# Kernel tuning notes

Measured on AMD Instinct MI355X. Metric: run time of the kernel, lower is better.

Reference implementation:

```python
import jax, jax.numpy as jnp
import numpy as np

B, T, C, H, D, E, K = 4, 1024, 1024, 16, 64, 8, 2
HID = 2 * D  # expert MLP hidden width (assumed 2*head_dim)
NEG = jnp.finfo(jnp.float32).min


def setup_inputs() -> dict:
    key = jax.random.key(0)
    ks = jax.random.split(key, 16)
    s = 0.02
    # rotary tables [max_pos, head_dim]
    inv_freq = 1.0 / (10000.0 ** (jnp.arange(0, D, 2, dtype=jnp.float32) / D))
    freqs = jnp.arange(T, dtype=jnp.float32)[:, None] * inv_freq[None, :]
    emb = jnp.concatenate([freqs, freqs], axis=-1)  # [T, D]
    return {
        "x": jax.random.normal(ks[0], (B, T, C), jnp.float32),
        "position_ids": jnp.sort(jax.random.randint(ks[1], (B, T), 0, T), axis=-1),
        "cos": jnp.cos(emb),
        "sin": jnp.sin(emb),
        "rq": s * jax.random.normal(ks[2], (D, E), jnp.float32),
        "rk": s * jax.random.normal(ks[3], (D, E), jnp.float32),
        "rv": s * jax.random.normal(ks[4], (D, E), jnp.float32),
        "q_w1": s * jax.random.normal(ks[5], (E, D, HID), jnp.float32),
        "q_w2": s * jax.random.normal(ks[6], (E, HID, D), jnp.float32),
        "k_w1": s * jax.random.normal(ks[7], (E, D, HID), jnp.float32),
        "k_w2": s * jax.random.normal(ks[8], (E, HID, D), jnp.float32),
        "v_w1": s * jax.random.normal(ks[9], (E, D, HID), jnp.float32),
        "v_w2": s * jax.random.normal(ks[10], (E, HID, D), jnp.float32),
        "o_w": s * jax.random.normal(ks[11], (C, C), jnp.float32),  # torch Linear weight [out,in]
    }


def _rotate_half(x):
    x1, x2 = x[..., : D // 2], x[..., D // 2:]
    return jnp.concatenate([-x2, x1], axis=-1)


def _moe_head_proj(xh, r_w, w1, w2):
    """Per-head top-k routed expert MLP. xh: [B,T,H,D]."""
    logits = jnp.einsum('bthd,de->bthe', xh, r_w)            # router logits
    vals, idx = jax.lax.top_k(logits, K)                     # [B,T,H,K]
    w = jax.nn.softmax(vals, axis=-1)
    onehot = jax.nn.one_hot(idx, E, dtype=xh.dtype)          # [B,T,H,K,E]
    w_full = jnp.einsum('bthk,bthke->bthe', w, onehot)       # scatter weights to all experts
    h = jax.nn.gelu(jnp.einsum('bthd,edf->bthef', xh, w1))   # all-expert hidden
    out = jnp.einsum('bthe,bthef,efg->bthg', w_full, h, w2)  # masked weighted combine
    return out, logits


def reference(x, position_ids, cos, sin, rq, rk, rv, q_w1, q_w2, k_w1, k_w2, v_w1, v_w2, o_w):
    xh = x.reshape(B, T, H, D)
    q, _ = _moe_head_proj(xh, rq, q_w1, q_w2)
    k, _ = _moe_head_proj(xh, rk, k_w1, k_w2)
    v, _ = _moe_head_proj(xh, rv, v_w1, v_w2)
    q = q.transpose(0, 2, 1, 3)  # [B,H,T,D]
    k = k.transpose(0, 2, 1, 3)
    v = v.transpose(0, 2, 1, 3)
    # RoPE
    c = cos[position_ids][:, None, :, :]  # [B,1,T,D]
    s = sin[position_ids][:, None, :, :]
    q = q * c + _rotate_half(q) * s
    k = k * c + _rotate_half(k) * s
    # causal SDPA
    scores = jnp.einsum('bhqd,bhkd->bhqk', q, k) / jnp.sqrt(jnp.float32(D))
    causal = jnp.tril(jnp.ones((T, T), dtype=bool))
    scores = jnp.where(causal, scores, NEG)
    attn = jax.nn.softmax(scores, axis=-1)
    out = jnp.einsum('bhqk,bhkd->bhqd', attn, v)
    out = out.transpose(0, 2, 1, 3).reshape(B, T, C)
    return out @ o_w.T
```

## Files before the change

kernel.cpp:

```cpp
#include <hip/hip_runtime.h>
#include <math.h>

#define BB 4
#define TT 1024
#define CCH 1024
#define HH 16
#define DD 64
#define EE 8
#define HID 128
#define CAP 8192
#define GEXP 504

typedef unsigned short u16;
typedef unsigned int u32;
typedef short bf16x8 __attribute__((ext_vector_type(8)));
typedef short bf16x4 __attribute__((ext_vector_type(4)));
typedef float f32x4 __attribute__((ext_vector_type(4)));

__device__ __forceinline__ u16 f2bf(float f) {
    unsigned int u = __float_as_uint(f);
    unsigned int r = (u + 0x7FFFu + ((u >> 16) & 1u)) >> 16;
    return (u16)r;
}
__device__ __forceinline__ u16 f2bf_f(float f) {
    return (u16)((__float_as_uint(f) + 0x8000u) >> 16);
}
__device__ __forceinline__ u32 pkbf(float lo, float hi) {
    u32 a = __float_as_uint(lo) + 0x8000u;
    u32 b = __float_as_uint(hi) + 0x8000u;
    return __builtin_amdgcn_perm(b, a, 0x07060302u);
}
__device__ __forceinline__ float gelu_fast(float z) {
    float t = z * z;
    float wn = __builtin_fmaf(t, -0.07135481283f, -1.5957691216f);
    float e = __expf(z * wn);
    return __fdividef(z, 1.f + e);
}

#define GLD16(gp, lp) __builtin_amdgcn_global_load_lds( \
    (const __attribute__((address_space(1))) u32*)(gp), \
    (__attribute__((address_space(3))) u32*)(lp), 16, 0, 0)

__global__ __launch_bounds__(256) void prep_kernel(
    const float* __restrict__ x,
    const float* __restrict__ rq, const float* __restrict__ rk, const float* __restrict__ rv,
    unsigned int* __restrict__ counts,
    unsigned int* __restrict__ idxbuf, float2* __restrict__ wtbuf,
    const float* __restrict__ qw1, const float* __restrict__ kw1, const float* __restrict__ vw1,
    const float* __restrict__ qw2, const float* __restrict__ kw2, const float* __restrict__ vw2,
    u16* __restrict__ img1, u16* __restrict__ img2,
    const float* __restrict__ ow, u16* __restrict__ owbf)
{
    const int bi = blockIdx.x;
    const int tid = threadIdx.x;

    if (bi < 192) {
        int t = bi * 256 + tid;
        if (t < 24576) {
            int c = t & 7, f = (t >> 3) & 127, e = (t >> 10) & 7, p = t >> 13;
            const float* w1 = ((p == 0) ? qw1 : (p == 1) ? kw1 : vw1) + e * 8192;
            int dbase = 8 * (c ^ (f & 7));
            u16 tmp[8];
            #pragma unroll
            for (int j = 0; j < 8; ++j) tmp[j] = f2bf(w1[(dbase + j) * 128 + f]);
            uint4 ov;
            ov.x = (u32)tmp[0] | ((u32)tmp[1] << 16);
            ov.y = (u32)tmp[2] | ((u32)tmp[3] << 16);
            ov.z = (u32)tmp[4] | ((u32)tmp[5] << 16);
            ov.w = (u32)tmp[6] | ((u32)tmp[7] << 16);
            ((uint4*)img1)[t] = ov;
        } else {
            int i = t - 24576;
            int m = i & 15, g = (i >> 4) & 63, e = (i >> 10) & 7, p = i >> 13;
            const float* w2 = ((p == 0) ? qw2 : (p == 1) ? kw2 : vw2) + e * 8192;
            u16* dstrow = img2 + (p * 8 + e) * 8192 + g * 128;
            #pragma unroll
            for (int u = 0; u < 2; ++u) {
                int gg = 2 * m + u;
                int fbase = 16 * (gg >> 2) + 4 * (gg & 3);
                int pos = gg ^ (g & 31);
                u16 a0 = f2bf(w2[(fbase + 0) * 64 + g]);
                u16 a1 = f2bf(w2[(fbase + 1) * 64 + g]);
                u16 a2 = f2bf(w2[(fbase + 2) * 64 + g]);
                u16 a3 = f2bf(w2[(fbase + 3) * 64 + g]);
                uint2 ov;
                ov.x = (u32)a0 | ((u32)a1 << 16);
                ov.y = (u32)a2 | ((u32)a3 << 16);
                *(uint2*)(dstrow + pos * 4) = ov;
            }
        }
        return;
    }

    if (bi < 1216) {
        int i = (bi - 192) * 256 + tid;
        float4 v = ((const float4*)ow)[i];
        unsigned int lov = (unsigned int)f2bf(v.x) | ((unsigned int)f2bf(v.y) << 16);
        unsigned int hiv = (unsigned int)f2bf(v.z) | ((unsigned int)f2bf(v.w) << 16);
        ((uint2*)owbf)[i] = make_uint2(lov, hiv);
        return;
    }

    {
        const unsigned int g = (bi - 1216) * 256 + tid;

        __shared__ float rS[3][64][8];
        __shared__ int lcnt[192];
        __shared__ int lbase[192];

        for (int i = tid; i < 1536; i += 256) {
            int p = i >> 9, rem = i & 511;
            const float* rp = (p == 0) ? rq : (p == 1) ? rk : rv;
            rS[p][rem >> 3][rem & 7] = rp[rem];
        }
        if (tid < 192) lcnt[tid] = 0;
        __syncthreads();

        float lg[3][8];
        #pragma unroll
        for (int p = 0; p < 3; ++p)
            #pragma unroll
            for (int e = 0; e < 8; ++e) lg[p][e] = 0.f;

        const float* xr = x + (size_t)g * 64;
        for (int i4 = 0; i4 < 16; ++i4) {
            float4 xv = ((const float4*)xr)[i4];
            float xa[4] = {xv.x, xv.y, xv.z, xv.w};
            #pragma unroll
            for (int m = 0; m < 4; ++m) {
                int d = i4 * 4 + m;
                #pragma unroll
                for (int p = 0; p < 3; ++p) {
                    float4 r0 = *(const float4*)&rS[p][d][0];
                    float4 r1 = *(const float4*)&rS[p][d][4];
                    lg[p][0] += xa[m] * r0.x; lg[p][1] += xa[m] * r0.y;
                    lg[p][2] += xa[m] * r0.z; lg[p][3] += xa[m] * r0.w;
                    lg[p][4] += xa[m] * r1.x; lg[p][5] += xa[m] * r1.y;
                    lg[p][6] += xa[m] * r1.z; lg[p][7] += xa[m] * r1.w;
                }
            }
        }

        int ppe[3]; float2 pw[3]; int slot[3];
        #pragma unroll
        for (int p = 0; p < 3; ++p) {
            int i1 = 0; float v1 = lg[p][0];
            #pragma unroll
            for (int e = 1; e < 8; ++e) { if (lg[p][e] > v1) { v1 = lg[p][e]; i1 = e; } }
            int i2 = -1; float v2 = -3.402823466e38f;
            #pragma unroll
            for (int e = 0; e < 8; ++e) { if (e != i1 && lg[p][e] > v2) { v2 = lg[p][e]; i2 = e; } }
            float z = __expf(v2 - v1);
            float inv = 1.f / (1.f + z);
            float wa = inv, wb = z * inv;
            int lo = min(i1, i2), hi = max(i1, i2);
            float wlo = (i1 < i2) ? wa : wb;
            float whi = (i1 < i2) ? wb : wa;
            int pel = p * 64 + lo * 8 + hi;
            ppe[p] = pel; pw[p] = make_float2(wlo, whi);
            slot[p] = atomicAdd(&lcnt[pel], 1);
        }
        __syncthreads();
        if (tid < 192) {
            int c = lcnt[tid];
            lbase[tid] = c ? (int)atomicAdd(&counts[tid], (unsigned int)c) : 0;
        }
        __syncthreads();
        #pragma unroll
        for (int p = 0; p < 3; ++p) {
            int pos = lbase[ppe[p]] + slot[p];
            if (pos < CAP) {
                idxbuf[ppe[p] * CAP + pos] = g;
                wtbuf[ppe[p] * CAP + pos]  = pw[p];
            }
        }
    }
}

__global__ __launch_bounds__(128) void sched_kernel(
    const unsigned int* __restrict__ counts, unsigned int* __restrict__ blockinfo)
{
    const int tid = threadIdx.x;
    __shared__ int nsub[84];
    __shared__ int extra[84];
    __shared__ int frac[84];
    __shared__ int alloc[84];
    __shared__ int startS[84];
    __shared__ int nnzS, totalS, rem2S;

    if (tid < 84) {
        int p = tid / 28, q = tid - 28 * p, lo = 0;
        while (q >= 7 - lo) { q -= 7 - lo; ++lo; }
        int hi = lo + 1 + q;
        int n = (int)counts[p * 64 + lo * 8 + hi];
        if (n > CAP) n = CAP;
        nsub[tid] = (n + 31) >> 5;
    }
    __syncthreads();
    if (tid == 0) {
        int tot = 0, nz = 0;
        for (int i = 0; i < 84; ++i) { tot += nsub[i]; nz += (nsub[i] > 0); }
        totalS = tot; nnzS = nz;
    }
    __syncthreads();
    const int R = GEXP - nnzS;
    if (tid < 84) {
        if (nsub[tid] > 0) {
            int e = (int)(((long long)nsub[tid] * R) / totalS);
            extra[tid] = e;
            frac[tid] = nsub[tid] * R - e * totalS;
        } else { extra[tid] = 0; frac[tid] = -1; }
    }
    __syncthreads();
    if (tid == 0) {
        int se = 0;
        for (int i = 0; i < 84; ++i) se += extra[i];
        rem2S = GEXP - nnzS - se;
    }
    __syncthreads();
    if (tid < 84) {
        if (nsub[tid] > 0) {
            int rank = 0;
            for (int j = 0; j < 84; ++j)
                if (nsub[j] > 0 && (frac[j] > frac[tid] || (frac[j] == frac[tid] && j < tid))) ++rank;
            alloc[tid] = 1 + extra[tid] + (rank < rem2S ? 1 : 0);
        } else alloc[tid] = 0;
    }
    __syncthreads();
    if (tid == 0) {
        int s = 0;
        for (int i = 0; i < 84; ++i) { startS[i] = s; s += alloc[i]; }
    }
    __syncthreads();
    if (tid < 84) {
        int a = alloc[tid], st = startS[tid];
        for (int c = 0; c < a; ++c)
            blockinfo[st + c] = (unsigned)tid | ((unsigned)c << 8) | ((unsigned)a << 20);
    }
}

__global__ __launch_bounds__(512, 2) void expert_kernel(
    const float* __restrict__ x, const int* __restrict__ pos_ids,
    const float* __restrict__ cosb, const float* __restrict__ sinb,
    const u16* __restrict__ img1, const u16* __restrict__ img2,
    const unsigned int* __restrict__ counts,
    const unsigned int* __restrict__ idxbuf, const float2* __restrict__ wtbuf,
    const unsigned int* __restrict__ blockinfo,
    u16* __restrict__ qb, u16* __restrict__ kb, u16* __restrict__ vb)
{
    const int tid = threadIdx.x;
    const unsigned int info = blockinfo[blockIdx.x];
    const int pe84 = info & 255;
    const int chunk = (info >> 8) & 0xFFF;
    const int nch = info >> 20;
    const int p = pe84 / 28;
    int q28 = pe84 - p * 28;
    int lo = 0;
    while (q28 >= 7 - lo) { q28 -= 7 - lo; ++lo; }
    const int hi = lo + 1 + q28;
    const int pe = p * 64 + lo * 8 + hi;

    int n = (int)counts[pe]; if (n == 0) return; if (n > CAP) n = CAP;

    u16* outp = (p == 0) ? qb : (p == 1) ? kb : vb;
    const unsigned int* il = idxbuf + pe * CAP;
    const float2* wl = wtbuf + pe * CAP;

    __shared__ __align__(16) u16 wsh[32768];

    {
        const u16* a0 = img1 + (p * 8 + lo) * 8192;
        const u16* b0 = img2 + (p * 8 + lo) * 8192;
        const u16* a1 = img1 + (p * 8 + hi) * 8192;
        const u16* b1 = img2 + (p * 8 + hi) * 8192;
        #pragma unroll
        for (int k = 0; k < 2; ++k) {
            int o = (k * 512 + tid) * 8;
            GLD16(a0 + o, wsh + o);
            GLD16(b0 + o, wsh + 8192 + o);
            GLD16(a1 + o, wsh + 16384 + o);
            GLD16(b1 + o, wsh + 24576 + o);
        }
    }
    __syncthreads();

    const int lane = tid & 63, w = tid >> 6, quad = lane >> 4, m16 = lane & 15;
    const int f7 = m16 & 7;
    const int wid = chunk * 8 + w;
    const int WRK = nch * 8;
    const int nsub = (n + 31) >> 5;

    for (int s = wid; s < nsub; s += WRK) {
        const int base = s * 32;
        unsigned int gtok = 0, obase = 0; float wlo_ = 0.f, whi_ = 0.f;
        int posv = 0, valid = 0;
        if (lane < 32) {
            int j = base + lane;
            valid = (j < n);
            int jc = valid ? j : (n - 1);
            gtok = il[jc];
            float2 wv = wl[jc];
            wlo_ = valid ? wv.x : 0.f; whi_ = valid ? wv.y : 0.f;
            unsigned int b_ = gtok >> 14, h_ = gtok & 15, t_ = (gtok >> 4) & 1023;
            obase = ((b_ * 16 + h_) * 1024 + t_) * 64;
            posv = pos_ids[b_ * 1024 + t_];
        }

        float wf00 = __shfl(wlo_, m16, 64);
        float wf10 = __shfl(whi_, m16, 64);
        float wf01 = __shfl(wlo_, 16 + m16, 64);
        float wf11 = __shfl(whi_, 16 + m16, 64);

        bf16x8 Afr[2][2];
        #pragma unroll
        for (int mt2 = 0; mt2 < 2; ++mt2) {
            unsigned int gm = (unsigned int)__shfl((int)gtok, mt2 * 16 + m16, 64);
            const float* xr = x + (size_t)gm * 64 + 8 * quad;
            float4 xa0 = *(const float4*)(xr);
            float4 xa1 = *(const float4*)(xr + 4);
            float4 xb0 = *(const float4*)(xr + 32);
            float4 xb1 = *(const float4*)(xr + 36);
            bf16x8 A0, A1;
            A0[0] = (short)f2bf_f(xa0.x); A0[1] = (short)f2bf_f(xa0.y);
            A0[2] = (short)f2bf_f(xa0.z); A0[3] = (short)f2bf_f(xa0.w);
            A0[4] = (short)f2bf_f(xa1.x); A0[5] = (short)f2bf_f(xa1.y);
            A0[6] = (short)f2bf_f(xa1.z); A0[7] = (short)f2bf_f(xa1.w);
            A1[0] = (short)f2bf_f(xb0.x); A1[1] = (short)f2bf_f(xb0.y);
            A1[2] = (short)f2bf_f(xb0.z); A1[3] = (short)f2bf_f(xb0.w);
            A1[4] = (short)f2bf_f(xb1.x); A1[5] = (short)f2bf_f(xb1.y);
            A1[6] = (short)f2bf_f(xb1.z); A1[7] = (short)f2bf_f(xb1.w);
            Afr[mt2][0] = A0; Afr[mt2][1] = A1;
        }

        f32x4 acc2[2][4];
        #pragma unroll
        for (int mt2 = 0; mt2 < 2; ++mt2)
            #pragma unroll
            for (int nt = 0; nt < 4; ++nt) acc2[mt2][nt] = (f32x4){0.f, 0.f, 0.f, 0.f};

        #pragma unroll 1
        for (int ekk = 0; ekk < 8; ++ekk) {
            const int e = ekk >> 2;
            const int kk = ekk & 3;
            const u16* w1b = wsh + e * 16384;
            const u16* w2b = w1b + 8192;
            const float wt0 = e ? wf10 : wf00;
            const float wt1 = e ? wf11 : wf01;

            f32x4 c[2][2];
            #pragma unroll
            for (int ntl = 0; ntl < 2; ++ntl) {
                const int f = 16 * (2 * kk + ntl) + m16;
                const u16* w1f = w1b + f * 64;
                bf16x8 wa = *(const bf16x8*)(w1f + (((quad    ) ^ f7) << 3));
                bf16x8 wb = *(const bf16x8*)(w1f + (((quad + 4) ^ f7) << 3));
                #pragma unroll
                for (int mt2 = 0; mt2 < 2; ++mt2) {
                    f32x4 t = (f32x4){0.f, 0.f, 0.f, 0.f};
                    t = __builtin_amdgcn_mfma_f32_16x16x32_bf16(wa, Afr[mt2][0], t, 0, 0, 0);
                    c[ntl][mt2] = __builtin_amdgcn_mfma_f32_16x16x32_bf16(wb, Afr[mt2][1], t, 0, 0, 0);
                }
            }

            bf16x4 w2f[2][4];
            #pragma unroll
            for (int ntl = 0; ntl < 2; ++ntl) {
                const int gg = 4 * (2 * kk + ntl) + quad;
                #pragma unroll
                for (int nt2 = 0; nt2 < 4; ++nt2) {
                    const int g = 16 * nt2 + m16;
                    const int pos = gg ^ (g & 31);
                    w2f[ntl][nt2] = *(const bf16x4*)(w2b + g * 128 + pos * 4);
                }
            }

            #pragma unroll
            for (int mt2 = 0; mt2 < 2; ++mt2) {
                const float wt = mt2 ? wt1 : wt0;
                #pragma unroll
                for (int ntl = 0; ntl < 2; ++ntl) {
                    float g0 = wt * gelu_fast(c[ntl][mt2][0]);
                    float g1 = wt * gelu_fast(c[ntl][mt2][1]);
                    float g2 = wt * gelu_fast(c[ntl][mt2][2]);
                    float g3 = wt * gelu_fast(c[ntl][mt2][3]);
                    union { u32 u[2]; bf16x4 v; } bf_;
                    bf_.u[0] = pkbf(g0, g1);
                    bf_.u[1] = pkbf(g2, g3);
                    #pragma unroll
                    for (int nt2 = 0; nt2 < 4; ++nt2)
                        acc2[mt2][nt2] = __builtin_amdgcn_mfma_f32_16x16x16bf16_1k(
                            w2f[ntl][nt2], bf_.v, acc2[mt2][nt2], 0, 0, 0);
                }
            }
        }

        #pragma unroll
        for (int mt2 = 0; mt2 < 2; ++mt2) {
            const int tk = mt2 * 16 + m16;
            int   pos_r = __shfl(posv, tk, 64);
            unsigned int ob = (unsigned int)__shfl((int)obase, tk, 64);
            int   val_r = __shfl(valid, tk, 64);
            if (p < 2) {
                #pragma unroll
                for (int ntp = 0; ntp < 2; ++ntp) {
                    const int d0 = 16 * ntp + 4 * quad;
                    float4 cv = *(const float4*)&cosb[pos_r * 64 + d0];
                    float4 sv = *(const float4*)&sinb[pos_r * 64 + d0];
                    float o1[4], o2[4];
                    #pragma unroll
                    for (int r = 0; r < 4; ++r) {
                        float v1 = acc2[mt2][ntp][r];
                        float v2 = acc2[mt2][ntp + 2][r];
                        float cd = (&cv.x)[r], sd = (&sv.x)[r];
                        o1[r] = v1 * cd - v2 * sd;
                        o2[r] = v2 * cd + v1 * sd;
                    }
                    if (val_r) {
                        uint2 s1, s2;
                        s1.x = (u32)f2bf(o1[0]) | ((u32)f2bf(o1[1]) << 16);
                        s1.y = (u32)f2bf(o1[2]) | ((u32)f2bf(o1[3]) << 16);
                        s2.x = (u32)f2bf(o2[0]) | ((u32)f2bf(o2[1]) << 16);
                        s2.y = (u32)f2bf(o2[2]) | ((u32)f2bf(o2[3]) << 16);
                        *(uint2*)&outp[ob + d0]      = s1;
                        *(uint2*)&outp[ob + d0 + 32] = s2;
                    }
                }
            } else {
                if (val_r) {
                    #pragma unroll
                    for (int nt2 = 0; nt2 < 4; ++nt2) {
                        uint2 s1;
                        s1.x = (u32)f2bf(acc2[mt2][nt2][0]) | ((u32)f2bf(acc2[mt2][nt2][1]) << 16);
                        s1.y = (u32)f2bf(acc2[mt2][nt2][2]) | ((u32)f2bf(acc2[mt2][nt2][3]) << 16);
                        *(uint2*)&outp[ob + 16 * nt2 + 4 * quad] = s1;
                    }
                }
            }
        }
    }
}

__global__ __launch_bounds__(256) void attn_kernel(
    const u16* __restrict__ qbp, const u16* __restrict__ kbp,
    const u16* __restrict__ vbp, u16* __restrict__ ao)
{
    const int tid = threadIdx.x;
    const int i8 = blockIdx.x & 7;
    const int plane_i = blockIdx.x >> 3;
    const int h = plane_i & 15, b = plane_i >> 4;
    const size_t plane = (size_t)plane_i * 1024 * 64;
    const u16* qp = qbp + plane;
    const u16* kp = kbp + plane;
    const u16* vp = vbp + plane;

    const int w = tid >> 6, lane = tid & 63, quad = lane >> 4, m16 = lane & 15;
    const int row = tid >> 2, seg = tid & 3;
    const int kjv = tid & 63, dgv = tid >> 6;

    __shared__ u16 Ks[64][72];
    __shared__ u16 Vt[64][72];
    __shared__ u16 Ps[4][16][72];

    #pragma unroll 1
    for (int half = 0; half < 2; ++half) {
        const int qt = half ? (15 - i8) : i8;
        const int q0 = qt * 64;

        const u16* qrow = &qp[(size_t)(q0 + 16 * w + m16) * 64 + 8 * quad];
        bf16x8 aq0 = *(const bf16x8*)(qrow);
        bf16x8 aq1 = *(const bf16x8*)(qrow + 32);

        uint4 kr0, kr1; ushort4 vr0, vr1, vr2, vr3;
        {
            const uint4* src = (const uint4*)&kp[(size_t)row * 64 + seg * 16];
            kr0 = src[0]; kr1 = src[1];
            const u16* vb2 = &vp[(size_t)kjv * 64 + dgv * 4];
            vr0 = *(const ushort4*)(vb2);
            vr1 = *(const ushort4*)(vb2 + 16);
            vr2 = *(const ushort4*)(vb2 + 32);
            vr3 = *(const ushort4*)(vb2 + 48);
        }

        float m_s = -1e30f, l_s = 0.f;
        f32x4 oacc[4];
        #pragma unroll
        for (int i = 0; i < 4; ++i) oacc[i] = (f32x4){0.f, 0.f, 0.f, 0.f};

        const int qrow_l = 16 * w + m16;

        for (int kt = 0; kt <= qt; ++kt) {
            __syncthreads();
            {
                uint4* dst = (uint4*)&Ks[row][seg * 16];
                dst[0] = kr0; dst[1] = kr1;
                int d0 = dgv * 4;
                Vt[d0 + 0][kjv] = vr0.x; Vt[d0 + 1][kjv] = vr0.y;
                Vt[d0 + 2][kjv] = vr0.z; Vt[d0 + 3][kjv] = vr0.w;
                Vt[d0 + 16][kjv] = vr1.x; Vt[d0 + 17][kjv] = vr1.y;
                Vt[d0 + 18][kjv] = vr1.z; Vt[d0 + 19][kjv] = vr1.w;
                Vt[d0 + 32][kjv] = vr2.x; Vt[d0 + 33][kjv] = vr2.y;
                Vt[d0 + 34][kjv] = vr2.z; Vt[d0 + 35][kjv] = vr2.w;
                Vt[d0 + 48][kjv] = vr3.x; Vt[d0 + 49][kjv] = vr3.y;
                Vt[d0 + 50][kjv] = vr3.z; Vt[d0 + 51][kjv] = vr3.w;
            }
            __syncthreads();
            if (kt < qt) {
                const int k0n = (kt + 1) * 64;
                const uint4* src = (const uint4*)&kp[(size_t)(k0n + row) * 64 + seg * 16];
                kr0 = src[0]; kr1 = src[1];
                const u16* vb2 = &vp[(size_t)(k0n + kjv) * 64 + dgv * 4];
                vr0 = *(const ushort4*)(vb2);
                vr1 = *(const ushort4*)(vb2 + 16);
                vr2 = *(const ushort4*)(vb2 + 32);
                vr3 = *(const ushort4*)(vb2 + 48);
            }

            f32x4 sv[4];
            #pragma unroll
            for (int ct = 0; ct < 4; ++ct) {
                bf16x8 bk0 = *(const bf16x8*)&Ks[16 * ct + m16][8 * quad];
                bf16x8 bk1 = *(const bf16x8*)&Ks[16 * ct + m16][32 + 8 * quad];
                f32x4 acc = (f32x4){0.f, 0.f, 0.f, 0.f};
                acc = __builtin_amdgcn_mfma_f32_16x16x32_bf16(bk0, aq0, acc, 0, 0, 0);
                acc = __builtin_amdgcn_mfma_f32_16x16x32_bf16(bk1, aq1, acc, 0, 0, 0);
                sv[ct] = acc;
            }

            float s[4][4];
            const bool diag = (kt == qt);
            #pragma unroll
            for (int ct = 0; ct < 4; ++ct)
                #pragma unroll
                for (int reg = 0; reg < 4; ++reg) {
                    float v = sv[ct][reg] * 0.125f;
                    if (diag) {
                        int krow = 16 * ct + 4 * quad + reg;
                        if (krow > qrow_l) v = -1e30f;
                    }
                    s[ct][reg] = v;
                }

            float rm = s[0][0];
            #pragma unroll
            for (int ct = 0; ct < 4; ++ct)
                #pragma unroll
                for (int reg = 0; reg < 4; ++reg) rm = fmaxf(rm, s[ct][reg]);
            rm = fmaxf(rm, __shfl_xor(rm, 16, 64));
            rm = fmaxf(rm, __shfl_xor(rm, 32, 64));
            float mn = fmaxf(m_s, rm);
            float al = __expf(m_s - mn);
            float sum = 0.f;
            #pragma unroll
            for (int ct = 0; ct < 4; ++ct)
                #pragma unroll
                for (int reg = 0; reg < 4; ++reg) {
                    float pv = __expf(s[ct][reg] - mn);
                    s[ct][reg] = pv;
                    sum += pv;
                }
            sum += __shfl_xor(sum, 16, 64);
            sum += __shfl_xor(sum, 32, 64);
            l_s = l_s * al + sum;
            m_s = mn;

            bf16x4 pt[4];
            #pragma unroll
            for (int ct = 0; ct < 4; ++ct) {
                union { u32 u[2]; bf16x4 v; } pb;
                pb.u[0] = pkbf(s[ct][0], s[ct][1]);
                pb.u[1] = pkbf(s[ct][2], s[ct][3]);
                pt[ct] = pb.v;
            }

            #pragma unroll
            for (int dt = 0; dt < 4; ++dt)
                #pragma unroll
                for (int reg = 0; reg < 4; ++reg) oacc[dt][reg] *= al;

            #pragma unroll
            for (int dt = 0; dt < 4; ++dt) {
                #pragma unroll
                for (int ct = 0; ct < 4; ++ct) {
                    bf16x4 vf = *(const bf16x4*)&Vt[16 * dt + m16][16 * ct + 4 * quad];
                    oacc[dt] = __builtin_amdgcn_mfma_f32_16x16x16bf16_1k(vf, pt[ct], oacc[dt], 0, 0, 0);
                }
            }
        }

        float linv = 1.f / l_s;
        #pragma unroll
        for (int dt = 0; dt < 4; ++dt) {
            u32 lo = (u32)f2bf(oacc[dt][0] * linv) | ((u32)f2bf(oacc[dt][1] * linv) << 16);
            u32 hi = (u32)f2bf(oacc[dt][2] * linv) | ((u32)f2bf(oacc[dt][3] * linv) << 16);
            *(u32*)&Ps[w][m16][16 * dt + 4 * quad]     = lo;
            *(u32*)&Ps[w][m16][16 * dt + 4 * quad + 2] = hi;
        }
        __syncthreads();
        #pragma unroll
        for (int reg = 0; reg < 4; ++reg) {
            int rw = q0 + 16 * w + 4 * quad + reg;
            size_t base = ((size_t)(b * 1024) + rw) * 1024 + h * 64;
            #pragma unroll
            for (int dt = 0; dt < 4; ++dt)
                ao[base + 16 * dt + m16] = Ps[w][4 * quad + reg][16 * dt + m16];
        }
    }
}

__global__ __launch_bounds__(256) void oproj_kernel(
    const u16* __restrict__ A, const u16* __restrict__ Bw,
    float* __restrict__ out)
{
    const int tid = threadIdx.x;
    const int bn = blockIdx.x & 7;
    const int bm = blockIdx.x >> 3;
    const int m0 = bm * 128, n0 = bn * 128;
    const int w = tid >> 6, lane = tid & 63, quad = lane >> 4, m16 = lane & 15;
    const int wm = (w >> 1) * 64, wn = (w & 1) * 64;

    __shared__ u16 As[128][32];
    __shared__ u16 Bs[128][32];

    f32x4 acc[4][4];
    #pragma unroll
    for (int mt = 0; mt < 4; ++mt)
        #pragma unroll
        for (int nt = 0; nt < 4; ++nt) acc[mt][nt] = (f32x4){0.f, 0.f, 0.f, 0.f};

    for (int k0 = 0; k0 < 1024; k0 += 32) {
        __syncthreads();
        {
            int rw = tid >> 1, sg = (tid & 1) * 16;
            const uint4* srcA = (const uint4*)&A[(size_t)(m0 + rw) * 1024 + k0 + sg];
            uint4 a0 = srcA[0], a1 = srcA[1];
            uint4* dstA = (uint4*)&As[rw][sg];
            dstA[0] = a0; dstA[1] = a1;
            const uint4* srcB = (const uint4*)&Bw[(size_t)(n0 + rw) * 1024 + k0 + sg];
            uint4 b0 = srcB[0], b1 = srcB[1];
            uint4* dstB = (uint4*)&Bs[rw][sg];
            dstB[0] = b0; dstB[1] = b1;
        }
        __syncthreads();
        bf16x8 af[4], bf_[4];
        #pragma unroll
        for (int mt = 0; mt < 4; ++mt) af[mt] = *(const bf16x8*)&As[wm + 16 * mt + m16][8 * quad];
        #pragma unroll
        for (int nt = 0; nt < 4; ++nt) bf_[nt] = *(const bf16x8*)&Bs[wn + 16 * nt + m16][8 * quad];
        #pragma unroll
        for (int mt = 0; mt < 4; ++mt)
            #pragma unroll
            for (int nt = 0; nt < 4; ++nt)
                acc[mt][nt] = __builtin_amdgcn_mfma_f32_16x16x32_bf16(af[mt], bf_[nt], acc[mt][nt], 0, 0, 0);
    }
    #pragma unroll
    for (int mt = 0; mt < 4; ++mt)
        #pragma unroll
        for (int nt = 0; nt < 4; ++nt)
            #pragma unroll
            for (int reg = 0; reg < 4; ++reg)
                out[(size_t)(m0 + wm + 16 * mt + 4 * quad + reg) * 1024 + n0 + wn + 16 * nt + m16] =
                    acc[mt][nt][reg];
}

extern "C" void kernel_launch(void* const* d_in, const int* in_sizes, int n_in,
                              void* d_out, int out_size, void* d_ws, size_t ws_size,
                              hipStream_t stream) {
    (void)in_sizes; (void)n_in; (void)out_size; (void)ws_size;
    const float* x    = (const float*)d_in[0];
    const int*   pid  = (const int*)  d_in[1];
    const float* cosb = (const float*)d_in[2];
    const float* sinb = (const float*)d_in[3];
    const float* rq   = (const float*)d_in[4];
    const float* rk   = (const float*)d_in[5];
    const float* rv   = (const float*)d_in[6];
    const float* qw1  = (const float*)d_in[7];
    const float* qw2  = (const float*)d_in[8];
    const float* kw1  = (const float*)d_in[9];
    const float* kw2  = (const float*)d_in[10];
    const float* vw1  = (const float*)d_in[11];
    const float* vw2  = (const float*)d_in[12];
    const float* ow   = (const float*)d_in[13];
    float* out = (float*)d_out;

    const size_t MB = 1u << 20;
    char* wsb = (char*)d_ws;
    u16* qb   = (u16*)(wsb + 0 * MB);
    u16* kb   = (u16*)(wsb + 8 * MB);
    u16* vb   = (u16*)(wsb + 16 * MB);
    u16* aobf = (u16*)(wsb + 24 * MB);
    u16* owbf = (u16*)(wsb + 32 * MB);
    unsigned int* idxbuf = (unsigned int*)(wsb + 34 * MB);
    float2*       wtbuf  = (float2*)(wsb + 41 * MB);
    unsigned int* counts = (unsigned int*)(wsb + 54 * MB);
    unsigned int* blockinfo = (unsigned int*)(wsb + 54 * MB + 4096);
    u16* w1img = (u16*)(wsb + 56 * MB);
    u16* w2img = (u16*)(wsb + 57 * MB);

    hipMemsetAsync(counts, 0, 1024, stream);

    hipLaunchKernelGGL(prep_kernel, dim3(1472), dim3(256), 0, stream,
                       x, rq, rk, rv, counts, idxbuf, wtbuf,
                       qw1, kw1, vw1, qw2, kw2, vw2, w1img, w2img,
                       ow, owbf);
    hipLaunchKernelGGL(sched_kernel, dim3(1), dim3(128), 0, stream,
                       counts, blockinfo);
    hipLaunchKernelGGL(expert_kernel, dim3(GEXP), dim3(512), 0, stream,
                       x, pid, cosb, sinb, w1img, w2img,
                       counts, idxbuf, wtbuf, blockinfo, qb, kb, vb);
    hipLaunchKernelGGL(attn_kernel, dim3(512), dim3(256), 0, stream,
                       qb, kb, vb, aobf);
    hipLaunchKernelGGL(oproj_kernel, dim3(256), dim3(256), 0, stream,
                       aobf, owbf, out);
}
```

Measured before the change: 229.2 us.

## Use exp2 in gelu/softmax, unroll expert loop, retile and prefetch output projection

Folds log2(e) into the GELU polynomial coefficients and the attention scale so exp2f can replace __expf, saving a multiply per exponential. The expert hidden-layer loop is unrolled by two. The output projection moves to 128x64 tiles with 512 blocks to fill more CUs, pads LDS rows to 40 elements to reduce bank conflicts, and register-prefetches the next K slice while the current one is computed. Smaller N tiles reduce per-block reuse, and the unrolling raises register pressure.

Result: slower. 234.9 us (+2.5%).

```diff
diff --git a/kernel.cpp b/kernel.cpp
--- a/kernel.cpp
+++ b/kernel.cpp
@@ -32,8 +32,8 @@
 }
 __device__ __forceinline__ float gelu_fast(float z) {
     float t = z * z;
-    float wn = __builtin_fmaf(t, -0.07135481283f, -1.5957691216f);
-    float e = __expf(z * wn);
+    float wn = __builtin_fmaf(t, -0.10294343f, -2.3022082f);
+    float e = exp2f(z * wn);
     return __fdividef(z, 1.f + e);
 }
 
@@ -338,7 +338,7 @@
             #pragma unroll
             for (int nt = 0; nt < 4; ++nt) acc2[mt2][nt] = (f32x4){0.f, 0.f, 0.f, 0.f};
 
-        #pragma unroll 1
+        #pragma unroll 2
         for (int ekk = 0; ekk < 8; ++ekk) {
             const int e = ekk >> 2;
             const int kk = ekk & 3;
@@ -532,7 +532,7 @@
             for (int ct = 0; ct < 4; ++ct)
                 #pragma unroll
                 for (int reg = 0; reg < 4; ++reg) {
-                    float v = sv[ct][reg] * 0.125f;
+                    float v = sv[ct][reg] * 0.18033688f;
                     if (diag) {
                         int krow = 16 * ct + 4 * quad + reg;
                         if (krow > qrow_l) v = -1e30f;
@@ -548,13 +548,13 @@
             rm = fmaxf(rm, __shfl_xor(rm, 16, 64));
             rm = fmaxf(rm, __shfl_xor(rm, 32, 64));
             float mn = fmaxf(m_s, rm);
-            float al = __expf(m_s - mn);
+            float al = exp2f(m_s - mn);
             float sum = 0.f;
             #pragma unroll
             for (int ct = 0; ct < 4; ++ct)
                 #pragma unroll
                 for (int reg = 0; reg < 4; ++reg) {
-                    float pv = __expf(s[ct][reg] - mn);
+                    float pv = exp2f(s[ct][reg] - mn);
                     s[ct][reg] = pv;
                     sum += pv;
                 }
@@ -612,50 +612,56 @@
     float* __restrict__ out)
 {
     const int tid = threadIdx.x;
-    const int bn = blockIdx.x & 7;
-    const int bm = blockIdx.x >> 3;
-    const int m0 = bm * 128, n0 = bn * 128;
+    const int bn = blockIdx.x & 15;
+    const int bm = blockIdx.x >> 4;
+    const int m0 = bm * 128, n0 = bn * 64;
     const int w = tid >> 6, lane = tid & 63, quad = lane >> 4, m16 = lane & 15;
-    const int wm = (w >> 1) * 64, wn = (w & 1) * 64;
-
-    __shared__ u16 As[128][32];
-    __shared__ u16 Bs[128][32];
-
-    f32x4 acc[4][4];
+    const int wm = (w >> 1) * 64, wn = (w & 1) * 32;
+
+    __shared__ u16 As[128][40];
+    __shared__ u16 Bs[64][40];
+
+    const int arw = tid >> 1, asg = (tid & 1) * 16;
+    const int brw = tid >> 2, bsg = (tid & 3) * 8;
+    const u16* srcA = A + (size_t)(m0 + arw) * 1024 + asg;
+    const u16* srcB = Bw + (size_t)(n0 + brw) * 1024 + bsg;
+
+    f32x4 acc[4][2];
     #pragma unroll
     for (int mt = 0; mt < 4; ++mt)
         #pragma unroll
-        for (int nt = 0; nt < 4; ++nt) acc[mt][nt] = (f32x4){0.f, 0.f, 0.f, 0.f};
+        for (int nt = 0; nt < 2; ++nt) acc[mt][nt] = (f32x4){0.f, 0.f, 0.f, 0.f};
+
+    uint4 pa0 = ((const uint4*)srcA)[0];
+    uint4 pa1 = ((const uint4*)srcA)[1];
+    uint4 pb0 = *(const uint4*)srcB;
 
     for (int k0 = 0; k0 < 1024; k0 += 32) {
         __syncthreads();
-        {
-            int rw = tid >> 1, sg = (tid & 1) * 16;
-            const uint4* srcA = (const uint4*)&A[(size_t)(m0 + rw) * 1024 + k0 + sg];
-            uint4 a0 = srcA[0], a1 = srcA[1];
-            uint4* dstA = (uint4*)&As[rw][sg];
-            dstA[0] = a0; dstA[1] = a1;
-            const uint4* srcB = (const uint4*)&Bw[(size_t)(n0 + rw) * 1024 + k0 + sg];
-            uint4 b0 = srcB[0], b1 = srcB[1];
-            uint4* dstB = (uint4*)&Bs[rw][sg];
-            dstB[0] = b0; dstB[1] = b1;
-        }
+        *(uint4*)&As[arw][asg]     = pa0;
+        *(uint4*)&As[arw][asg + 8] = pa1;
+        *(uint4*)&Bs[brw][bsg]     = pb0;
         __syncthreads();
-        bf16x8 af[4], bf_[4];
+        if (k0 + 32 < 1024) {
+            pa0 = ((const uint4*)(srcA + k0 + 32))[0];
+            pa1 = ((const uint4*)(srcA + k0 + 32))[1];
+            pb0 = *(const uint4*)(srcB + k0 + 32);
+        }
+        bf16x8 af[4], bfr[2];
         #pragma unroll
         for (int mt = 0; mt < 4; ++mt) af[mt] = *(const bf16x8*)&As[wm + 16 * mt + m16][8 * quad];
         #pragma unroll
-        for (int nt = 0; nt < 4; ++nt) bf_[nt] = *(const bf16x8*)&Bs[wn + 16 * nt + m16][8 * quad];
+        for (int nt = 0; nt < 2; ++nt) bfr[nt] = *(const bf16x8*)&Bs[wn + 16 * nt + m16][8 * quad];
         #pragma unroll
         for (int mt = 0; mt < 4; ++mt)
             #pragma unroll
-            for (int nt = 0; nt < 4; ++nt)
-                acc[mt][nt] = __builtin_amdgcn_mfma_f32_16x16x32_bf16(af[mt], bf_[nt], acc[mt][nt], 0, 0, 0);
+            for (int nt = 0; nt < 2; ++nt)
+                acc[mt][nt] = __builtin_amdgcn_mfma_f32_16x16x32_bf16(af[mt], bfr[nt], acc[mt][nt], 0, 0, 0);
     }
     #pragma unroll
     for (int mt = 0; mt < 4; ++mt)
         #pragma unroll
-        for (int nt = 0; nt < 4; ++nt)
+        for (int nt = 0; nt < 2; ++nt)
             #pragma unroll
             for (int reg = 0; reg < 4; ++reg)
                 out[(size_t)(m0 + wm + 16 * mt + 4 * quad + reg) * 1024 + n0 + wn + 16 * nt + m16] =
@@ -709,6 +715,6 @@
                        counts, idxbuf, wtbuf, blockinfo, qb, kb, vb);
     hipLaunchKernelGGL(attn_kernel, dim3(512), dim3(256), 0, stream,
                        qb, kb, vb, aobf);
-    hipLaunchKernelGGL(oproj_kernel, dim3(256), dim3(256), 0, stream,
+    hipLaunchKernelGGL(oproj_kernel, dim3(512), dim3(256), 0, stream,
                        aobf, owbf, out);
 }
```
